# Performance work log

Hardware: AMD Instinct MI355X
Metric: run time of the kernel (lower is better)

The kernel has to match this reference:

```python
import jax, jax.numpy as jnp
import numpy as np

# Four fixed 3x3 'gradient' kernels (left, right, up, down), stacked as OIHW (4,1,3,3).
_K = np.zeros((4, 1, 3, 3), np.float32)
_K[0, 0, 1, 0] = -1.0; _K[0, 0, 1, 1] = 1.0   # left:  center - left neighbor
_K[1, 0, 1, 1] = 1.0;  _K[1, 0, 1, 2] = -1.0  # right: center - right neighbor
_K[2, 0, 0, 1] = -1.0; _K[2, 0, 1, 1] = 1.0   # up:    center - upper neighbor
_K[3, 0, 1, 1] = 1.0;  _K[3, 0, 2, 1] = -1.0  # down:  center - lower neighbor
KERNELS = jnp.asarray(_K)

LOSS_WEIGHT = 1.0
POOL = 4


def _avgpool4(x):
    # AvgPool2d(4) on NCHW with H,W divisible by 4
    b, c, h, w = x.shape
    return x.reshape(b, c, h // POOL, POOL, w // POOL, POOL).mean(axis=(3, 5))


def _grad_conv(x):
    # F.conv2d(x, kernels, padding=1); x: (B,1,Hp,Wp) -> (B,4,Hp,Wp)
    return jax.lax.conv_general_dilated(
        x, KERNELS, window_strides=(1, 1), padding=((1, 1), (1, 1)),
        dimension_numbers=('NCHW', 'OIHW', 'NCHW'))


def setup_inputs() -> dict:
    key = jax.random.key(0)
    k1, k2 = jax.random.split(key)
    B, C, H, W = 32, 3, 512, 512
    x = jax.random.uniform(k1, (B, C, H, W), dtype=jnp.float32)
    pred = jax.random.uniform(k2, (B, C, H, W), dtype=jnp.float32)
    return {"x": x, "pred": pred}


def reference(x, pred):
    # channel mean -> (B,1,H,W), then 4x4 average pool -> (B,1,H/4,W/4)
    org_pool = _avgpool4(jnp.mean(x, axis=1, keepdims=True))
    enh_pool = _avgpool4(jnp.mean(pred, axis=1, keepdims=True))
    # NOTE: the original computes weight_diff and E_1 but never uses them in the
    # returned loss, so they are omitted (no effect on output or gradients).
    d = _grad_conv(org_pool) - _grad_conv(enh_pool)  # (B,4,Hp,Wp)
    # mean(D_left + D_right + D_up + D_down) == mean over (B,Hp,Wp) of channel-sum
    E = jnp.mean(jnp.sum(d * d, axis=1))
    return LOSS_WEIGHT * E
```

## Files before the change

kernel.cpp:

```cpp
#include <hip/hip_runtime.h>

constexpr int B  = 32;
constexpr int C  = 3;
constexpr int H  = 512;
constexpr int W  = 512;
constexpr int HP = H / 4;
constexpr int WP = W / 4;
constexpr int NP = B * HP * WP;

constexpr int TS = 32;
constexpr int HS = TS + 2;
constexpr int TILES_PER_IMG = (HP / TS) * (WP / TS);
constexpr int NBLOCKS = B * TILES_PER_IMG;

__global__ __launch_bounds__(256) void spatial_loss_fused(
        const float* __restrict__ x,
        const float* __restrict__ pred,
        float* __restrict__ out) {
    __shared__ float pt[HS][HS + 1];

    int blk = blockIdx.x;
    int b   = blk >> 4;
    int ty  = (blk >> 2) & 3;
    int tx  = blk & 3;
    int tid = threadIdx.x;

    for (int i = tid; i < HS * HS; i += 256) {
        int hy = i / HS;
        int hx = i - hy * HS;
        int gy = ty * TS + hy - 1;
        int gx = tx * TS + hx - 1;
        float s = 0.0f;
        if ((unsigned)gy < (unsigned)HP && (unsigned)gx < (unsigned)WP) {
            size_t base = (((size_t)b * C) * H + (size_t)gy * 4) * W + (size_t)gx * 4;
            #pragma unroll
            for (int c = 0; c < C; ++c) {
                const float4* xb = (const float4*)(x    + base + (size_t)c * H * W);
                const float4* pb = (const float4*)(pred + base + (size_t)c * H * W);
                #pragma unroll
                for (int r = 0; r < 4; ++r) {
                    float4 xv = xb[r * (W / 4)];
                    float4 pv = pb[r * (W / 4)];
                    s += (xv.x - pv.x) + (xv.y - pv.y) + (xv.z - pv.z) + (xv.w - pv.w);
                }
            }
            s *= (1.0f / 48.0f);
        }
        pt[hy][hx] = s;
    }
    __syncthreads();

    float acc = 0.0f;
    #pragma unroll
    for (int j = 0; j < (TS * TS) / 256; ++j) {
        int i  = tid + j * 256;
        int iy = i >> 5;
        int ix = i & 31;
        float c = pt[iy + 1][ix + 1];
        float l = pt[iy + 1][ix + 0];
        float r = pt[iy + 1][ix + 2];
        float u = pt[iy + 0][ix + 1];
        float d = pt[iy + 2][ix + 1];
        float g0 = c - l, g1 = c - r, g2 = c - u, g3 = c - d;
        acc += g0 * g0 + g1 * g1 + g2 * g2 + g3 * g3;
    }

    #pragma unroll
    for (int off = 32; off > 0; off >>= 1)
        acc += __shfl_down(acc, off, 64);

    __shared__ float ws_red[4];
    int lane = tid & 63;
    int wid  = tid >> 6;
    if (lane == 0) ws_red[wid] = acc;
    __syncthreads();
    if (tid == 0) {
        float s = ws_red[0] + ws_red[1] + ws_red[2] + ws_red[3];
        atomicAdd(out, s * (1.0f / (float)NP));
    }
}

extern "C" void kernel_launch(void* const* d_in, const int* in_sizes, int n_in,
                              void* d_out, int out_size, void* d_ws, size_t ws_size,
                              hipStream_t stream) {
    const float* x    = (const float*)d_in[0];
    const float* pred = (const float*)d_in[1];
    float* out = (float*)d_out;

    hipMemsetAsync(out, 0, sizeof(float), stream);

    spatial_loss_fused<<<NBLOCKS, 256, 0, stream>>>(x, pred, out);
}
```

Baseline: 220.7 us.

## Exploit gradient symmetry to shrink halo and use wider 64x32 tiles

The left/right and up/down gradient terms are squared differences of the same neighbour pairs, so each interior difference is counted twice, with separate handling for the zero-padded image boundaries. This removes the need for a right and bottom halo, leaving a one-sided halo on wider 64x32 tiles. That cuts redundant halo loads of x and pred, which dominate the memory-bound kernel. The cost is boundary special-casing logic and fewer blocks (256 instead of 512), which may reduce occupancy.

```diff
diff --git a/kernel.cpp b/kernel.cpp
--- a/kernel.cpp
+++ b/kernel.cpp
@@ -8,28 +8,33 @@
 constexpr int WP = W / 4;
 constexpr int NP = B * HP * WP;
 
-constexpr int TS = 32;
-constexpr int HS = TS + 2;
-constexpr int TILES_PER_IMG = (HP / TS) * (WP / TS);
-constexpr int NBLOCKS = B * TILES_PER_IMG;
+constexpr int TX = 64;
+constexpr int TY = 32;
+constexpr int HX = TX + 1;
+constexpr int HY = TY + 1;
+constexpr int TILES_X = WP / TX;
+constexpr int TILES_Y = HP / TY;
+constexpr int NBLOCKS = B * TILES_X * TILES_Y;
 
 __global__ __launch_bounds__(256) void spatial_loss_fused(
         const float* __restrict__ x,
         const float* __restrict__ pred,
         float* __restrict__ out) {
-    __shared__ float pt[HS][HS + 1];
+    __shared__ float pt[HY][HX];
 
     int blk = blockIdx.x;
-    int b   = blk >> 4;
-    int ty  = (blk >> 2) & 3;
-    int tx  = blk & 3;
+    int b   = blk >> 3;
+    int ty  = (blk >> 1) & 3;
+    int tx  = blk & 1;
+    int y0  = ty * TY;
+    int x0  = tx * TX;
     int tid = threadIdx.x;
 
-    for (int i = tid; i < HS * HS; i += 256) {
-        int hy = i / HS;
-        int hx = i - hy * HS;
-        int gy = ty * TS + hy - 1;
-        int gx = tx * TS + hx - 1;
+    for (int i = tid; i < HY * HX; i += 256) {
+        int hy = i / HX;
+        int hx = i - hy * HX;
+        int gy = y0 + hy - 1;
+        int gx = x0 + hx - 1;
         float s = 0.0f;
         if ((unsigned)gy < (unsigned)HP && (unsigned)gx < (unsigned)WP) {
             size_t base = (((size_t)b * C) * H + (size_t)gy * 4) * W + (size_t)gx * 4;
@@ -52,17 +57,22 @@
 
     float acc = 0.0f;
     #pragma unroll
-    for (int j = 0; j < (TS * TS) / 256; ++j) {
+    for (int j = 0; j < (TY * TX) / 256; ++j) {
         int i  = tid + j * 256;
-        int iy = i >> 5;
-        int ix = i & 31;
-        float c = pt[iy + 1][ix + 1];
-        float l = pt[iy + 1][ix + 0];
-        float r = pt[iy + 1][ix + 2];
-        float u = pt[iy + 0][ix + 1];
-        float d = pt[iy + 2][ix + 1];
-        float g0 = c - l, g1 = c - r, g2 = c - u, g3 = c - d;
-        acc += g0 * g0 + g1 * g1 + g2 * g2 + g3 * g3;
+        int r  = i >> 6;
+        int xx = i & 63;
+        int gy = y0 + r;
+        int gx = x0 + xx;
+        float c  = pt[r + 1][xx + 1];
+        float up = pt[r + 0][xx + 1];
+        float lf = pt[r + 1][xx + 0];
+        float dy = c - up;
+        float dx = c - lf;
+        float wy = (gy > 0) ? 2.0f : 1.0f;
+        float wx = (gx > 0) ? 2.0f : 1.0f;
+        acc += wy * dy * dy + wx * dx * dx;
+        if (gy == HP - 1) acc += c * c;
+        if (gx == WP - 1) acc += c * c;
     }
 
     #pragma unroll
```

Result: no change. 219.5 us (-0.5%).
